# Performance work log

Measured on AMD Instinct MI355X. Metric: run time of the kernel, lower is better.

The kernel has to match this reference:

```python
import jax, jax.numpy as jnp
import numpy as np

N_NODES = 100000
N_EDGES = 800000
FEATURE_DIM = 128
DEPTH = 3


def setup_inputs() -> dict:
    key = jax.random.key(0)
    k1, k2, k3 = jax.random.split(key, 3)
    x = jax.random.normal(k1, (N_NODES, FEATURE_DIM), dtype=jnp.float32)
    edge_index = jax.random.randint(k2, (2, N_EDGES), 0, N_NODES, dtype=jnp.int32)
    W = jax.random.normal(k3, (FEATURE_DIM, FEATURE_DIM), dtype=jnp.float32) * (1.0 / np.sqrt(FEATURE_DIM))
    b = jnp.zeros((FEATURE_DIM,), dtype=jnp.float32)
    return {"x": x, "edge_index": edge_index, "W": W, "b": b}


def reference(x, edge_index, W, b):
    n = x.shape[0]
    # PyG GCNConv default: add self-loops, symmetric normalization
    loop = jnp.arange(n, dtype=edge_index.dtype)
    src = jnp.concatenate([edge_index[0], loop])  # [E+N]
    dst = jnp.concatenate([edge_index[1], loop])  # [E+N]
    ones = jnp.ones(src.shape[0], dtype=x.dtype)
    deg = jax.ops.segment_sum(ones, dst, num_segments=n)  # in-degree incl. self-loop
    dis = jnp.where(deg > 0, jax.lax.rsqrt(deg), 0.0)  # deg^{-1/2}
    norm = (dis[src] * dis[dst])[:, None]  # [E+N, 1]

    # depth iterations share the SAME conv weights (time-invariant)
    for _ in range(DEPTH):
        h = x @ W  # [N, D] linear transform first (PyG order)
        msg = h[src] * norm  # gather + normalize, [E+N, D]
        agg = jax.ops.segment_sum(msg, dst, num_segments=n)  # scatter-add
        x = jax.nn.relu(agg + b)  # bias, NullControl adds 0, dropout_rate=0 is identity
    return x
```

## Files before the change

kernel.cpp:

```cpp
#include <hip/hip_runtime.h>

#define FD 128
#define CAP 64

typedef __attribute__((ext_vector_type(8))) short short8;
typedef __attribute__((ext_vector_type(4))) float floatx4;

__device__ inline unsigned short f2bf(float f) {
  unsigned u = __float_as_uint(f);
  u += 0x7fffu + ((u >> 16) & 1u);
  return (unsigned short)(u >> 16);
}
__device__ inline float lo16f(unsigned v) { return __uint_as_float(v << 16); }
__device__ inline float hi16f(unsigned v) { return __uint_as_float(v & 0xffff0000u); }
__device__ inline int imin(int a, int b) { return a < b ? a : b; }
__device__ inline unsigned umin(unsigned a, unsigned b) { return a < b ? a : b; }

__global__ __launch_bounds__(256) void k_prep(const float* __restrict__ W,
                                              short* __restrict__ whi,
                                              int* __restrict__ cursor, int N,
                                              int zB) {
  int b = blockIdx.x;
  if (b < zB) {
    int i = b * 256 + threadIdx.x;
    if (i < N) cursor[i] = 0;
  } else {
    int idx = (b - zB) * 256 + threadIdx.x;
    int j = idx & 7, lane = (idx >> 3) & 63, kt = (idx >> 9) & 3, ct = idx >> 11;
    int k = kt * 32 + (lane >> 4) * 8 + j;
    int n = ct * 16 + (lane & 15);
    whi[idx] = (short)f2bf(W[k * FD + n]);
  }
}

__global__ __launch_bounds__(256) void k_fill(const int* __restrict__ src,
                                              const int* __restrict__ dst,
                                              int* __restrict__ cursor,
                                              int* __restrict__ buck, int E) {
  int e = blockIdx.x * 256 + threadIdx.x;
  if (e < E) {
    int d = dst[e], s = src[e];
    int pos = atomicAdd(&cursor[d], 1);
    if (pos < CAP) buck[(size_t)d * CAP + pos] = s;
  }
}

template <bool ABF16>
__global__ __launch_bounds__(256) void k_gemm(const void* __restrict__ Av,
                                              const short* __restrict__ Wf_hi,
                                              const int* __restrict__ cursor,
                                              unsigned short* __restrict__ H, int N) {
  __shared__ short whi[FD * FD];
  int tid = threadIdx.x;
#pragma unroll
  for (int it = 0; it < 8; ++it) {
    int idx = (it * 256 + tid) * 8;
    *(short8*)&whi[idx] = *(const short8*)&Wf_hi[idx];
  }
  __syncthreads();

  int wid = tid >> 6, lane = tid & 63;
  int quad = lane >> 4, m = lane & 15;
  int rbase = blockIdx.x * 128 + wid * 32;

  short8 ahi[2][4];
#pragma unroll
  for (int t = 0; t < 2; ++t) {
    int arow = rbase + t * 16 + m;
    if (arow >= N) arow = N - 1;
    if (ABF16) {
      const unsigned short* ap = (const unsigned short*)Av + (size_t)arow * FD;
#pragma unroll
      for (int kt = 0; kt < 4; ++kt)
        ahi[t][kt] = *(const short8*)(ap + kt * 32 + quad * 8);
    } else {
      const float* ap = (const float*)Av + (size_t)arow * FD;
#pragma unroll
      for (int kt = 0; kt < 4; ++kt) {
        const float* p = ap + kt * 32 + quad * 8;
        float4 a0 = *(const float4*)p;
        float4 a1 = *(const float4*)(p + 4);
        ahi[t][kt][0] = (short)f2bf(a0.x); ahi[t][kt][1] = (short)f2bf(a0.y);
        ahi[t][kt][2] = (short)f2bf(a0.z); ahi[t][kt][3] = (short)f2bf(a0.w);
        ahi[t][kt][4] = (short)f2bf(a1.x); ahi[t][kt][5] = (short)f2bf(a1.y);
        ahi[t][kt][6] = (short)f2bf(a1.z); ahi[t][kt][7] = (short)f2bf(a1.w);
      }
    }
  }

  float dis0[4], dis1[4];
#pragma unroll
  for (int r = 0; r < 4; ++r) {
    int row0 = imin(rbase + quad * 4 + r, N - 1);
    int row1 = imin(rbase + 16 + quad * 4 + r, N - 1);
    dis0[r] = rsqrtf((float)(imin(cursor[row0], CAP) + 1));
    dis1[r] = rsqrtf((float)(imin(cursor[row1], CAP) + 1));
  }

#pragma unroll
  for (int ct = 0; ct < 8; ++ct) {
    floatx4 acc0 = {0.f, 0.f, 0.f, 0.f}, acc1 = {0.f, 0.f, 0.f, 0.f};
#pragma unroll
    for (int kt = 0; kt < 4; ++kt) {
      int fo = (((ct << 2) + kt) * 64 + lane) * 8;
      short8 bhi = *(const short8*)&whi[fo];
      acc0 = __builtin_amdgcn_mfma_f32_16x16x32_bf16(ahi[0][kt], bhi, acc0, 0, 0, 0);
      acc1 = __builtin_amdgcn_mfma_f32_16x16x32_bf16(ahi[1][kt], bhi, acc1, 0, 0, 0);
    }
#pragma unroll
    for (int r = 0; r < 4; ++r) {
      int row0 = rbase + quad * 4 + r;
      int row1 = rbase + 16 + quad * 4 + r;
      if (row0 < N) H[(size_t)row0 * FD + ct * 16 + m] = f2bf(acc0[r] * dis0[r]);
      if (row1 < N) H[(size_t)row1 * FD + ct * 16 + m] = f2bf(acc1[r] * dis1[r]);
    }
  }
}

template <bool OUTBF16>
__global__ __launch_bounds__(256) void k_agg(const unsigned int* __restrict__ h,
                                             const int* __restrict__ cursor,
                                             const int* __restrict__ buck,
                                             const float* __restrict__ bias,
                                             void* __restrict__ out, int N) {
  int wid = __builtin_amdgcn_readfirstlane(threadIdx.x >> 6);
  int lane = threadIdx.x & 63;
  int i = blockIdx.x * 4 + wid;
  if (i >= N) return;
  int deg = imin(cursor[i], CAP);
  float disi = rsqrtf((float)(deg + 1));
  unsigned v = h[(size_t)i * 64 + lane];
  float a0 = lo16f(v), a1 = hi16f(v);
  float b0 = 0.f, b1 = 0.f, c0 = 0.f, c1 = 0.f, d0 = 0.f, d1 = 0.f;

  const int4* bp = (const int4*)(buck + (size_t)i * CAP);
  int niter = (deg + 7) >> 3;
  for (int it = 0; it < niter; ++it) {
    int4 sa = bp[2 * it];
    int4 sb = bp[2 * it + 1];
    int srcs[8] = {sa.x, sa.y, sa.z, sa.w, sb.x, sb.y, sb.z, sb.w};
    unsigned g[8];
#pragma unroll
    for (int j = 0; j < 8; ++j) {
      unsigned su = (unsigned)__builtin_amdgcn_readfirstlane(srcs[j]);
      su = umin(su, (unsigned)(N - 1));
      g[j] = h[(size_t)su * 64 + lane];
    }
    int done = it * 8;
#pragma unroll
    for (int j = 0; j < 8; ++j) {
      float w = (done + j < deg) ? 1.f : 0.f;
      float l = lo16f(g[j]), hh = hi16f(g[j]);
      if (j == 0 || j == 4) { a0 = fmaf(w, l, a0); a1 = fmaf(w, hh, a1); }
      else if (j == 1 || j == 5) { b0 = fmaf(w, l, b0); b1 = fmaf(w, hh, b1); }
      else if (j == 2 || j == 6) { c0 = fmaf(w, l, c0); c1 = fmaf(w, hh, c1); }
      else { d0 = fmaf(w, l, d0); d1 = fmaf(w, hh, d1); }
    }
  }

  float2 bb = ((const float2*)bias)[lane];
  float o0 = fmaxf(fmaf(disi, (a0 + b0) + (c0 + d0), bb.x), 0.f);
  float o1 = fmaxf(fmaf(disi, (a1 + b1) + (c1 + d1), bb.y), 0.f);
  if (OUTBF16) {
    unsigned pk = ((unsigned)f2bf(o1) << 16) | (unsigned)f2bf(o0);
    ((unsigned*)out)[(size_t)i * 64 + lane] = pk;
  } else {
    ((float2*)out)[(size_t)i * 64 + lane] = make_float2(o0, o1);
  }
}


extern "C" void kernel_launch(void* const* d_in, const int* in_sizes, int n_in,
                              void* d_out, int out_size, void* d_ws, size_t ws_size,
                              hipStream_t stream) {
  const float* x = (const float*)d_in[0];
  const int* ei = (const int*)d_in[1];
  const float* Wg = (const float*)d_in[2];
  const float* b = (const float*)d_in[3];
  int N = in_sizes[0] / FD;
  int E = in_sizes[1] / 2;
  const int* src = ei;
  const int* dst = ei + E;

  char* p = (char*)d_ws;
  auto alloc = [&](size_t bytes) {
    void* r = (void*)p;
    p += (bytes + 255) & ~(size_t)255;
    return r;
  };
  int* cursor = (int*)alloc((size_t)N * 4);
  int* buck = (int*)alloc((size_t)N * CAP * 4);
  unsigned short* h = (unsigned short*)alloc((size_t)N * FD * 2);
  unsigned short* xb = (unsigned short*)alloc((size_t)N * FD * 2);
  short* wf_hi = (short*)alloc((size_t)FD * FD * 2);

  int zB = (N + 255) / 256;
  int wB = FD * FD / 256;
  int gG = (N + 127) / 128;
  int gA = (N + 3) / 4;
  int gE = (E + 255) / 256;

  k_prep<<<zB + wB, 256, 0, stream>>>(Wg, wf_hi, cursor, N, zB);
  k_fill<<<gE, 256, 0, stream>>>(src, dst, cursor, buck, E);

  k_gemm<false><<<gG, 256, 0, stream>>>(x, wf_hi, cursor, h, N);
  k_agg<true><<<gA, 256, 0, stream>>>((const unsigned*)h, cursor, buck, b, xb, N);
  k_gemm<true><<<gG, 256, 0, stream>>>(xb, wf_hi, cursor, h, N);
  k_agg<true><<<gA, 256, 0, stream>>>((const unsigned*)h, cursor, buck, b, xb, N);
  k_gemm<true><<<gG, 256, 0, stream>>>(xb, wf_hi, cursor, h, N);
  k_agg<false><<<gA, 256, 0, stream>>>((const unsigned*)h, cursor, buck, b, d_out, N);
}
```

Measured before the change: 295.3 us.

## Fuse edge bucketing with first GEMM and move source scaling into aggregation

Merges the edge-bucketing kernel and the first unscaled GEMM into one launch, so the two independent workloads can run concurrently on different blocks. Because the first GEMM no longer knows degrees, the first aggregation applies the source-degree normalization per edge by loading each source's cursor. This trades one launch and a serial dependency for extra scattered cursor loads and rsqrt work in the first aggregation pass. The GEMM blocks also allocate large shared memory, which may limit how many fill blocks run alongside them.

Result: no change. 296.0 us (+0.2%).

```diff
diff --git a/kernel.cpp b/kernel.cpp
--- a/kernel.cpp
+++ b/kernel.cpp
@@ -33,23 +33,12 @@
   }
 }
 
-__global__ __launch_bounds__(256) void k_fill(const int* __restrict__ src,
-                                              const int* __restrict__ dst,
-                                              int* __restrict__ cursor,
-                                              int* __restrict__ buck, int E) {
-  int e = blockIdx.x * 256 + threadIdx.x;
-  if (e < E) {
-    int d = dst[e], s = src[e];
-    int pos = atomicAdd(&cursor[d], 1);
-    if (pos < CAP) buck[(size_t)d * CAP + pos] = s;
-  }
-}
-
-template <bool ABF16>
-__global__ __launch_bounds__(256) void k_gemm(const void* __restrict__ Av,
-                                              const short* __restrict__ Wf_hi,
-                                              const int* __restrict__ cursor,
-                                              unsigned short* __restrict__ H, int N) {
+template <bool ABF16, bool SCALED>
+__device__ __forceinline__ void gemm_body(const void* __restrict__ Av,
+                                          const short* __restrict__ Wf_hi,
+                                          const int* __restrict__ cursor,
+                                          unsigned short* __restrict__ H,
+                                          int N, int bid) {
   __shared__ short whi[FD * FD];
   int tid = threadIdx.x;
 #pragma unroll
@@ -61,7 +50,7 @@
 
   int wid = tid >> 6, lane = tid & 63;
   int quad = lane >> 4, m = lane & 15;
-  int rbase = blockIdx.x * 128 + wid * 32;
+  int rbase = bid * 128 + wid * 32;
 
   short8 ahi[2][4];
 #pragma unroll
@@ -89,12 +78,14 @@
   }
 
   float dis0[4], dis1[4];
-#pragma unroll
-  for (int r = 0; r < 4; ++r) {
-    int row0 = imin(rbase + quad * 4 + r, N - 1);
-    int row1 = imin(rbase + 16 + quad * 4 + r, N - 1);
-    dis0[r] = rsqrtf((float)(imin(cursor[row0], CAP) + 1));
-    dis1[r] = rsqrtf((float)(imin(cursor[row1], CAP) + 1));
+  if constexpr (SCALED) {
+#pragma unroll
+    for (int r = 0; r < 4; ++r) {
+      int row0 = imin(rbase + quad * 4 + r, N - 1);
+      int row1 = imin(rbase + 16 + quad * 4 + r, N - 1);
+      dis0[r] = rsqrtf((float)(imin(cursor[row0], CAP) + 1));
+      dis1[r] = rsqrtf((float)(imin(cursor[row1], CAP) + 1));
+    }
   }
 
 #pragma unroll
@@ -111,13 +102,44 @@
     for (int r = 0; r < 4; ++r) {
       int row0 = rbase + quad * 4 + r;
       int row1 = rbase + 16 + quad * 4 + r;
-      if (row0 < N) H[(size_t)row0 * FD + ct * 16 + m] = f2bf(acc0[r] * dis0[r]);
-      if (row1 < N) H[(size_t)row1 * FD + ct * 16 + m] = f2bf(acc1[r] * dis1[r]);
-    }
-  }
-}
-
-template <bool OUTBF16>
+      if constexpr (SCALED) {
+        if (row0 < N) H[(size_t)row0 * FD + ct * 16 + m] = f2bf(acc0[r] * dis0[r]);
+        if (row1 < N) H[(size_t)row1 * FD + ct * 16 + m] = f2bf(acc1[r] * dis1[r]);
+      } else {
+        if (row0 < N) H[(size_t)row0 * FD + ct * 16 + m] = f2bf(acc0[r]);
+        if (row1 < N) H[(size_t)row1 * FD + ct * 16 + m] = f2bf(acc1[r]);
+      }
+    }
+  }
+}
+
+template <bool ABF16>
+__global__ __launch_bounds__(256) void k_gemm(const void* __restrict__ Av,
+                                              const short* __restrict__ Wf_hi,
+                                              const int* __restrict__ cursor,
+                                              unsigned short* __restrict__ H, int N) {
+  gemm_body<ABF16, true>(Av, Wf_hi, cursor, H, N, blockIdx.x);
+}
+
+__global__ __launch_bounds__(256) void k_fill_gemm(
+    const float* __restrict__ x, const short* __restrict__ Wf_hi,
+    const int* __restrict__ src, const int* __restrict__ dst,
+    int* __restrict__ cursor, int* __restrict__ buck,
+    unsigned short* __restrict__ H, int N, int E, int gG) {
+  int b = blockIdx.x;
+  if (b < gG) {
+    gemm_body<false, false>(x, Wf_hi, nullptr, H, N, b);
+  } else {
+    int e = (b - gG) * 256 + threadIdx.x;
+    if (e < E) {
+      int d = dst[e], s = src[e];
+      int pos = atomicAdd(&cursor[d], 1);
+      if (pos < CAP) buck[(size_t)d * CAP + pos] = s;
+    }
+  }
+}
+
+template <bool OUTBF16, bool SRCDIS>
 __global__ __launch_bounds__(256) void k_agg(const unsigned int* __restrict__ h,
                                              const int* __restrict__ cursor,
                                              const int* __restrict__ buck,
@@ -130,7 +152,8 @@
   int deg = imin(cursor[i], CAP);
   float disi = rsqrtf((float)(deg + 1));
   unsigned v = h[(size_t)i * 64 + lane];
-  float a0 = lo16f(v), a1 = hi16f(v);
+  float wself = SRCDIS ? disi : 1.f;
+  float a0 = wself * lo16f(v), a1 = wself * hi16f(v);
   float b0 = 0.f, b1 = 0.f, c0 = 0.f, c1 = 0.f, d0 = 0.f, d1 = 0.f;
 
   const int4* bp = (const int4*)(buck + (size_t)i * CAP);
@@ -140,21 +163,29 @@
     int4 sb = bp[2 * it + 1];
     int srcs[8] = {sa.x, sa.y, sa.z, sa.w, sb.x, sb.y, sb.z, sb.w};
     unsigned g[8];
+    int cs[8];
 #pragma unroll
     for (int j = 0; j < 8; ++j) {
       unsigned su = (unsigned)__builtin_amdgcn_readfirstlane(srcs[j]);
       su = umin(su, (unsigned)(N - 1));
       g[j] = h[(size_t)su * 64 + lane];
+      if (SRCDIS) cs[j] = cursor[su];
     }
     int done = it * 8;
 #pragma unroll
     for (int j = 0; j < 8; ++j) {
-      float w = (done + j < deg) ? 1.f : 0.f;
+      float wj;
+      if (SRCDIS) {
+        float ds = rsqrtf((float)(imin(cs[j], CAP) + 1));
+        wj = (done + j < deg) ? ds : 0.f;
+      } else {
+        wj = (done + j < deg) ? 1.f : 0.f;
+      }
       float l = lo16f(g[j]), hh = hi16f(g[j]);
-      if (j == 0 || j == 4) { a0 = fmaf(w, l, a0); a1 = fmaf(w, hh, a1); }
-      else if (j == 1 || j == 5) { b0 = fmaf(w, l, b0); b1 = fmaf(w, hh, b1); }
-      else if (j == 2 || j == 6) { c0 = fmaf(w, l, c0); c1 = fmaf(w, hh, c1); }
-      else { d0 = fmaf(w, l, d0); d1 = fmaf(w, hh, d1); }
+      if (j == 0 || j == 4) { a0 = fmaf(wj, l, a0); a1 = fmaf(wj, hh, a1); }
+      else if (j == 1 || j == 5) { b0 = fmaf(wj, l, b0); b1 = fmaf(wj, hh, b1); }
+      else if (j == 2 || j == 6) { c0 = fmaf(wj, l, c0); c1 = fmaf(wj, hh, c1); }
+      else { d0 = fmaf(wj, l, d0); d1 = fmaf(wj, hh, d1); }
     }
   }
 
@@ -201,12 +232,12 @@
   int gE = (E + 255) / 256;
 
   k_prep<<<zB + wB, 256, 0, stream>>>(Wg, wf_hi, cursor, N, zB);
-  k_fill<<<gE, 256, 0, stream>>>(src, dst, cursor, buck, E);
-
-  k_gemm<false><<<gG, 256, 0, stream>>>(x, wf_hi, cursor, h, N);
-  k_agg<true><<<gA, 256, 0, stream>>>((const unsigned*)h, cursor, buck, b, xb, N);
+  k_fill_gemm<<<gG + gE, 256, 0, stream>>>(x, wf_hi, src, dst, cursor, buck, h,
+                                           N, E, gG);
+
+  k_agg<true, true><<<gA, 256, 0, stream>>>((const unsigned*)h, cursor, buck, b, xb, N);
   k_gemm<true><<<gG, 256, 0, stream>>>(xb, wf_hi, cursor, h, N);
-  k_agg<true><<<gA, 256, 0, stream>>>((const unsigned*)h, cursor, buck, b, xb, N);
+  k_agg<true, false><<<gA, 256, 0, stream>>>((const unsigned*)h, cursor, buck, b, xb, N);
   k_gemm<true><<<gG, 256, 0, stream>>>(xb, wf_hi, cursor, h, N);
-  k_agg<false><<<gA, 256, 0, stream>>>((const unsigned*)h, cursor, buck, b, d_out, N);
-}
+  k_agg<false, false><<<gA, 256, 0, stream>>>((const unsigned*)h, cursor, buck, b, d_out, N);
+}
```

## Fuse aggregation with next layer's GEMM via LDS-staged tiles

Applied to the files above, without the earlier changes.

Replaces the middle agg+gemm kernel pairs with one fused kernel. Each 512-thread block aggregates 128 nodes (16 per wave, serially) into a swizzled LDS tile, then runs the MFMA transform on that tile and writes the next layer's normalized bf16 features. This removes the bf16 intermediate round-trip and two kernel launches, and it prefetches bucket indices for the next node. In exchange each wave walks 16 nodes in sequence, so there are fewer independent waves to hide gather latency, and LDS use grows to 64KB per block, which limits occupancy.

New measurement: 342.9 us. +16.1%, slower.

```diff
diff --git a/kernel.cpp b/kernel.cpp
--- a/kernel.cpp
+++ b/kernel.cpp
@@ -45,11 +45,10 @@
   }
 }
 
-template <bool ABF16>
-__global__ __launch_bounds__(256) void k_gemm(const void* __restrict__ Av,
-                                              const short* __restrict__ Wf_hi,
-                                              const int* __restrict__ cursor,
-                                              unsigned short* __restrict__ H, int N) {
+__global__ __launch_bounds__(256) void k_gemm1(const float* __restrict__ A,
+                                               const short* __restrict__ Wf_hi,
+                                               const int* __restrict__ cursor,
+                                               unsigned short* __restrict__ H, int N) {
   __shared__ short whi[FD * FD];
   int tid = threadIdx.x;
 #pragma unroll
@@ -68,23 +67,16 @@
   for (int t = 0; t < 2; ++t) {
     int arow = rbase + t * 16 + m;
     if (arow >= N) arow = N - 1;
-    if (ABF16) {
-      const unsigned short* ap = (const unsigned short*)Av + (size_t)arow * FD;
-#pragma unroll
-      for (int kt = 0; kt < 4; ++kt)
-        ahi[t][kt] = *(const short8*)(ap + kt * 32 + quad * 8);
-    } else {
-      const float* ap = (const float*)Av + (size_t)arow * FD;
-#pragma unroll
-      for (int kt = 0; kt < 4; ++kt) {
-        const float* p = ap + kt * 32 + quad * 8;
-        float4 a0 = *(const float4*)p;
-        float4 a1 = *(const float4*)(p + 4);
-        ahi[t][kt][0] = (short)f2bf(a0.x); ahi[t][kt][1] = (short)f2bf(a0.y);
-        ahi[t][kt][2] = (short)f2bf(a0.z); ahi[t][kt][3] = (short)f2bf(a0.w);
-        ahi[t][kt][4] = (short)f2bf(a1.x); ahi[t][kt][5] = (short)f2bf(a1.y);
-        ahi[t][kt][6] = (short)f2bf(a1.z); ahi[t][kt][7] = (short)f2bf(a1.w);
-      }
+    const float* ap = A + (size_t)arow * FD;
+#pragma unroll
+    for (int kt = 0; kt < 4; ++kt) {
+      const float* p = ap + kt * 32 + quad * 8;
+      float4 a0 = *(const float4*)p;
+      float4 a1 = *(const float4*)(p + 4);
+      ahi[t][kt][0] = (short)f2bf(a0.x); ahi[t][kt][1] = (short)f2bf(a0.y);
+      ahi[t][kt][2] = (short)f2bf(a0.z); ahi[t][kt][3] = (short)f2bf(a0.w);
+      ahi[t][kt][4] = (short)f2bf(a1.x); ahi[t][kt][5] = (short)f2bf(a1.y);
+      ahi[t][kt][6] = (short)f2bf(a1.z); ahi[t][kt][7] = (short)f2bf(a1.w);
     }
   }
 
@@ -117,12 +109,132 @@
   }
 }
 
-template <bool OUTBF16>
-__global__ __launch_bounds__(256) void k_agg(const unsigned int* __restrict__ h,
-                                             const int* __restrict__ cursor,
-                                             const int* __restrict__ buck,
-                                             const float* __restrict__ bias,
-                                             void* __restrict__ out, int N) {
+__global__ __launch_bounds__(512) void k_fused(const unsigned* __restrict__ h_in,
+                                               const int* __restrict__ cursor,
+                                               const int* __restrict__ buck,
+                                               const float* __restrict__ bias,
+                                               const short* __restrict__ Wf_hi,
+                                               unsigned short* __restrict__ H,
+                                               int N) {
+  __shared__ short whi[FD * FD];
+  __shared__ unsigned alds[128 * 64];
+  int tid = threadIdx.x;
+#pragma unroll
+  for (int it = 0; it < 4; ++it) {
+    int idx = (it * 512 + tid) * 8;
+    *(short8*)&whi[idx] = *(const short8*)&Wf_hi[idx];
+  }
+  int wid = tid >> 6, lane = tid & 63;
+  int rbase = blockIdx.x * 128;
+  int nbase = rbase + wid * 16;
+
+  int4 psa, psb;
+  int pdeg;
+  {
+    int node = nbase;
+    if (node < N) {
+      pdeg = imin(cursor[node], CAP);
+      const int4* bp = (const int4*)(buck + (size_t)node * CAP);
+      psa = bp[0];
+      psb = bp[1];
+    } else {
+      pdeg = -1;
+      psa = psb = make_int4(0, 0, 0, 0);
+    }
+  }
+  for (int n = 0; n < 16; ++n) {
+    int node = nbase + n;
+    int4 sa = psa, sb = psb;
+    int deg = __builtin_amdgcn_readfirstlane(pdeg);
+    if (n < 15) {
+      int nn = nbase + n + 1;
+      if (nn < N) {
+        pdeg = imin(cursor[nn], CAP);
+        const int4* bp = (const int4*)(buck + (size_t)nn * CAP);
+        psa = bp[0];
+        psb = bp[1];
+      } else {
+        pdeg = -1;
+      }
+    }
+    unsigned outw = 0;
+    if (deg >= 0) {
+      float disi = rsqrtf((float)(deg + 1));
+      unsigned v = h_in[(size_t)node * 64 + lane];
+      float a0 = lo16f(v), a1 = hi16f(v);
+      float b0 = 0.f, b1 = 0.f, c0 = 0.f, c1 = 0.f, d0 = 0.f, d1 = 0.f;
+      const int4* bp = (const int4*)(buck + (size_t)node * CAP);
+      int niter = (deg + 7) >> 3;
+      for (int it = 0; it < niter; ++it) {
+        if (it) {
+          sa = bp[2 * it];
+          sb = bp[2 * it + 1];
+        }
+        int srcs[8] = {sa.x, sa.y, sa.z, sa.w, sb.x, sb.y, sb.z, sb.w};
+        unsigned g[8];
+#pragma unroll
+        for (int j = 0; j < 8; ++j) {
+          unsigned su = (unsigned)__builtin_amdgcn_readfirstlane(srcs[j]);
+          su = umin(su, (unsigned)(N - 1));
+          g[j] = h_in[(size_t)su * 64 + lane];
+        }
+        int done = it * 8;
+#pragma unroll
+        for (int j = 0; j < 8; ++j) {
+          float w = (done + j < deg) ? 1.f : 0.f;
+          float l = lo16f(g[j]), hh = hi16f(g[j]);
+          if (j == 0 || j == 4) { a0 = fmaf(w, l, a0); a1 = fmaf(w, hh, a1); }
+          else if (j == 1 || j == 5) { b0 = fmaf(w, l, b0); b1 = fmaf(w, hh, b1); }
+          else if (j == 2 || j == 6) { c0 = fmaf(w, l, c0); c1 = fmaf(w, hh, c1); }
+          else { d0 = fmaf(w, l, d0); d1 = fmaf(w, hh, d1); }
+        }
+      }
+      float2 bb = ((const float2*)bias)[lane];
+      float o0 = fmaxf(fmaf(disi, (a0 + b0) + (c0 + d0), bb.x), 0.f);
+      float o1 = fmaxf(fmaf(disi, (a1 + b1) + (c1 + d1), bb.y), 0.f);
+      outw = ((unsigned)f2bf(o1) << 16) | (unsigned)f2bf(o0);
+    }
+    int lrow = wid * 16 + n;
+    alds[lrow * 64 + (((lane >> 2) ^ (lrow & 7)) << 2) + (lane & 3)] = outw;
+  }
+  __syncthreads();
+
+  int quad = lane >> 4, m = lane & 15;
+  int lrow = wid * 16 + m;
+  short8 ahi[4];
+#pragma unroll
+  for (int kt = 0; kt < 4; ++kt) {
+    int chunk = ((kt << 2) + quad) ^ (lrow & 7);
+    ahi[kt] = *(const short8*)&alds[lrow * 64 + chunk * 4];
+  }
+  float dis[4];
+#pragma unroll
+  for (int r = 0; r < 4; ++r) {
+    int row = imin(nbase + quad * 4 + r, N - 1);
+    dis[r] = rsqrtf((float)(imin(cursor[row], CAP) + 1));
+  }
+#pragma unroll
+  for (int ct = 0; ct < 8; ++ct) {
+    floatx4 acc = {0.f, 0.f, 0.f, 0.f};
+#pragma unroll
+    for (int kt = 0; kt < 4; ++kt) {
+      int fo = (((ct << 2) + kt) * 64 + lane) * 8;
+      short8 bhi = *(const short8*)&whi[fo];
+      acc = __builtin_amdgcn_mfma_f32_16x16x32_bf16(ahi[kt], bhi, acc, 0, 0, 0);
+    }
+#pragma unroll
+    for (int r = 0; r < 4; ++r) {
+      int row = nbase + quad * 4 + r;
+      if (row < N) H[(size_t)row * FD + ct * 16 + m] = f2bf(acc[r] * dis[r]);
+    }
+  }
+}
+
+__global__ __launch_bounds__(256) void k_agg_out(const unsigned int* __restrict__ h,
+                                                 const int* __restrict__ cursor,
+                                                 const int* __restrict__ buck,
+                                                 const float* __restrict__ bias,
+                                                 float2* __restrict__ out, int N) {
   int wid = __builtin_amdgcn_readfirstlane(threadIdx.x >> 6);
   int lane = threadIdx.x & 63;
   int i = blockIdx.x * 4 + wid;
@@ -161,12 +273,7 @@
   float2 bb = ((const float2*)bias)[lane];
   float o0 = fmaxf(fmaf(disi, (a0 + b0) + (c0 + d0), bb.x), 0.f);
   float o1 = fmaxf(fmaf(disi, (a1 + b1) + (c1 + d1), bb.y), 0.f);
-  if (OUTBF16) {
-    unsigned pk = ((unsigned)f2bf(o1) << 16) | (unsigned)f2bf(o0);
-    ((unsigned*)out)[(size_t)i * 64 + lane] = pk;
-  } else {
-    ((float2*)out)[(size_t)i * 64 + lane] = make_float2(o0, o1);
-  }
+  out[(size_t)i * 64 + lane] = make_float2(o0, o1);
 }
 
 
@@ -190,8 +297,8 @@
   };
   int* cursor = (int*)alloc((size_t)N * 4);
   int* buck = (int*)alloc((size_t)N * CAP * 4);
-  unsigned short* h = (unsigned short*)alloc((size_t)N * FD * 2);
-  unsigned short* xb = (unsigned short*)alloc((size_t)N * FD * 2);
+  unsigned short* h1 = (unsigned short*)alloc((size_t)N * FD * 2);
+  unsigned short* h2 = (unsigned short*)alloc((size_t)N * FD * 2);
   short* wf_hi = (short*)alloc((size_t)FD * FD * 2);
 
   int zB = (N + 255) / 256;
@@ -203,10 +310,9 @@
   k_prep<<<zB + wB, 256, 0, stream>>>(Wg, wf_hi, cursor, N, zB);
   k_fill<<<gE, 256, 0, stream>>>(src, dst, cursor, buck, E);
 
-  k_gemm<false><<<gG, 256, 0, stream>>>(x, wf_hi, cursor, h, N);
-  k_agg<true><<<gA, 256, 0, stream>>>((const unsigned*)h, cursor, buck, b, xb, N);
-  k_gemm<true><<<gG, 256, 0, stream>>>(xb, wf_hi, cursor, h, N);
-  k_agg<true><<<gA, 256, 0, stream>>>((const unsigned*)h, cursor, buck, b, xb, N);
-  k_gemm<true><<<gG, 256, 0, stream>>>(xb, wf_hi, cursor, h, N);
-  k_agg<false><<<gA, 256, 0, stream>>>((const unsigned*)h, cursor, buck, b, d_out, N);
-}
+  k_gemm1<<<gG, 256, 0, stream>>>(x, wf_hi, cursor, h1, N);
+  k_fused<<<gG, 512, 0, stream>>>((const unsigned*)h1, cursor, buck, b, wf_hi, h2, N);
+  k_fused<<<gG, 512, 0, stream>>>((const unsigned*)h2, cursor, buck, b, wf_hi, h1, N);
+  k_agg_out<<<gA, 256, 0, stream>>>((const unsigned*)h1, cursor, buck, b,
+                                    (float2*)d_out, N);
+}
```

## Process four nodes per wavefront in aggregation to raise memory-level parallelism

Applied to the files above, without the earlier changes.

The aggregation kernel now assigns four destination nodes to each wavefront instead of one. It issues the first eight neighbor gathers for all four nodes up front, then loops over any remaining neighbor chunks, so more independent loads are in flight per wave. The cost is higher register pressure, fewer waves in the grid, and padded gathers for low-degree nodes.

Measured after the change: 302.3 us. 1.02x slower.

```diff
diff --git a/kernel.cpp b/kernel.cpp
--- a/kernel.cpp
+++ b/kernel.cpp
@@ -123,49 +123,110 @@
                                              const int* __restrict__ buck,
                                              const float* __restrict__ bias,
                                              void* __restrict__ out, int N) {
-  int wid = __builtin_amdgcn_readfirstlane(threadIdx.x >> 6);
+  int wid = threadIdx.x >> 6;
   int lane = threadIdx.x & 63;
-  int i = blockIdx.x * 4 + wid;
-  if (i >= N) return;
-  int deg = imin(cursor[i], CAP);
-  float disi = rsqrtf((float)(deg + 1));
-  unsigned v = h[(size_t)i * 64 + lane];
-  float a0 = lo16f(v), a1 = hi16f(v);
-  float b0 = 0.f, b1 = 0.f, c0 = 0.f, c1 = 0.f, d0 = 0.f, d1 = 0.f;
-
-  const int4* bp = (const int4*)(buck + (size_t)i * CAP);
-  int niter = (deg + 7) >> 3;
-  for (int it = 0; it < niter; ++it) {
-    int4 sa = bp[2 * it];
-    int4 sb = bp[2 * it + 1];
-    int srcs[8] = {sa.x, sa.y, sa.z, sa.w, sb.x, sb.y, sb.z, sb.w};
-    unsigned g[8];
+  int base = blockIdx.x * 16 + wid * 4;
+  if (base >= N) return;
+
+  int node[4];
+#pragma unroll
+  for (int q = 0; q < 4; ++q) node[q] = imin(base + q, N - 1);
+
+  int degl[4];
+  int4 sa[4], sb[4];
+  unsigned v[4];
+#pragma unroll
+  for (int q = 0; q < 4; ++q) {
+    degl[q] = cursor[node[q]];
+    const int4* bp = (const int4*)(buck + (size_t)node[q] * CAP);
+    sa[q] = bp[0];
+    sb[q] = bp[1];
+    v[q] = h[(size_t)node[q] * 64 + lane];
+  }
+
+  unsigned g[4][8];
+#pragma unroll
+  for (int q = 0; q < 4; ++q) {
+    int srcs[8] = {sa[q].x, sa[q].y, sa[q].z, sa[q].w,
+                   sb[q].x, sb[q].y, sb[q].z, sb[q].w};
 #pragma unroll
     for (int j = 0; j < 8; ++j) {
       unsigned su = (unsigned)__builtin_amdgcn_readfirstlane(srcs[j]);
       su = umin(su, (unsigned)(N - 1));
-      g[j] = h[(size_t)su * 64 + lane];
-    }
-    int done = it * 8;
+      g[q][j] = h[(size_t)su * 64 + lane];
+    }
+  }
+
+  int deg[4], nit[4];
+  int nmax = 0;
+#pragma unroll
+  for (int q = 0; q < 4; ++q) {
+    deg[q] = __builtin_amdgcn_readfirstlane(imin(degl[q], CAP));
+    nit[q] = (deg[q] + 7) >> 3;
+    nmax = nit[q] > nmax ? nit[q] : nmax;
+  }
+
+  float s0[4], s1[4], t0[4], t1[4];
+#pragma unroll
+  for (int q = 0; q < 4; ++q) {
+    s0[q] = lo16f(v[q]); s1[q] = hi16f(v[q]);
+    t0[q] = 0.f; t1[q] = 0.f;
 #pragma unroll
     for (int j = 0; j < 8; ++j) {
-      float w = (done + j < deg) ? 1.f : 0.f;
-      float l = lo16f(g[j]), hh = hi16f(g[j]);
-      if (j == 0 || j == 4) { a0 = fmaf(w, l, a0); a1 = fmaf(w, hh, a1); }
-      else if (j == 1 || j == 5) { b0 = fmaf(w, l, b0); b1 = fmaf(w, hh, b1); }
-      else if (j == 2 || j == 6) { c0 = fmaf(w, l, c0); c1 = fmaf(w, hh, c1); }
-      else { d0 = fmaf(w, l, d0); d1 = fmaf(w, hh, d1); }
+      float w = (j < deg[q]) ? 1.f : 0.f;
+      float l = lo16f(g[q][j]), hh = hi16f(g[q][j]);
+      if (j & 1) { t0[q] = fmaf(w, l, t0[q]); t1[q] = fmaf(w, hh, t1[q]); }
+      else       { s0[q] = fmaf(w, l, s0[q]); s1[q] = fmaf(w, hh, s1[q]); }
+    }
+  }
+
+  for (int it = 1; it < nmax; ++it) {
+    unsigned gg[4][8];
+#pragma unroll
+    for (int q = 0; q < 4; ++q) {
+      if (it < nit[q]) {
+        const int4* bp = (const int4*)(buck + (size_t)node[q] * CAP);
+        int4 ta = bp[2 * it];
+        int4 tb = bp[2 * it + 1];
+        int srcs[8] = {ta.x, ta.y, ta.z, ta.w, tb.x, tb.y, tb.z, tb.w};
+#pragma unroll
+        for (int j = 0; j < 8; ++j) {
+          unsigned su = (unsigned)__builtin_amdgcn_readfirstlane(srcs[j]);
+          su = umin(su, (unsigned)(N - 1));
+          gg[q][j] = h[(size_t)su * 64 + lane];
+        }
+      } else {
+#pragma unroll
+        for (int j = 0; j < 8; ++j) gg[q][j] = 0;
+      }
+    }
+#pragma unroll
+    for (int q = 0; q < 4; ++q) {
+      int done = it * 8;
+#pragma unroll
+      for (int j = 0; j < 8; ++j) {
+        float w = (done + j < deg[q]) ? 1.f : 0.f;
+        float l = lo16f(gg[q][j]), hh = hi16f(gg[q][j]);
+        if (j & 1) { t0[q] = fmaf(w, l, t0[q]); t1[q] = fmaf(w, hh, t1[q]); }
+        else       { s0[q] = fmaf(w, l, s0[q]); s1[q] = fmaf(w, hh, s1[q]); }
+      }
     }
   }
 
   float2 bb = ((const float2*)bias)[lane];
-  float o0 = fmaxf(fmaf(disi, (a0 + b0) + (c0 + d0), bb.x), 0.f);
-  float o1 = fmaxf(fmaf(disi, (a1 + b1) + (c1 + d1), bb.y), 0.f);
-  if (OUTBF16) {
-    unsigned pk = ((unsigned)f2bf(o1) << 16) | (unsigned)f2bf(o0);
-    ((unsigned*)out)[(size_t)i * 64 + lane] = pk;
-  } else {
-    ((float2*)out)[(size_t)i * 64 + lane] = make_float2(o0, o1);
+#pragma unroll
+  for (int q = 0; q < 4; ++q) {
+    if (base + q < N) {
+      float disi = rsqrtf((float)(deg[q] + 1));
+      float o0 = fmaxf(fmaf(disi, s0[q] + t0[q], bb.x), 0.f);
+      float o1 = fmaxf(fmaf(disi, s1[q] + t1[q], bb.y), 0.f);
+      if (OUTBF16) {
+        unsigned pk = ((unsigned)f2bf(o1) << 16) | (unsigned)f2bf(o0);
+        ((unsigned*)out)[(size_t)(base + q) * 64 + lane] = pk;
+      } else {
+        ((float2*)out)[(size_t)(base + q) * 64 + lane] = make_float2(o0, o1);
+      }
+    }
   }
 }
 
@@ -197,7 +258,7 @@
   int zB = (N + 255) / 256;
   int wB = FD * FD / 256;
   int gG = (N + 127) / 128;
-  int gA = (N + 3) / 4;
+  int gA = (N + 15) / 16;
   int gE = (E + 255) / 256;
 
   k_prep<<<zB + wB, 256, 0, stream>>>(Wg, wf_hi, cursor, N, zB);
```
